# Kernel optimization log

Measured on AMD Instinct MI355X. Metric: run time of the kernel, lower is better.

The kernel has to match this reference:

```python
import jax, jax.numpy as jnp
import numpy as np

B, N, DIM = 16, 1024, 512
H, DH = 8, 64
INNER = H * DH            # 512
FF = 4 * DIM              # 2048
CIN = 2 * DIM             # conv inner dim = dim*expansion_factor = 1024
K = 31                    # depthwise kernel size
MAXPOS = 512
EPS = 1e-5


def layernorm(x, g, b):
    mu = jnp.mean(x, axis=-1, keepdims=True)
    var = jnp.mean(jnp.square(x - mu), axis=-1, keepdims=True)
    return (x - mu) * jax.lax.rsqrt(var + EPS) * g + b


def swish(x):
    return x * jax.nn.sigmoid(x)


def feed_forward(x, w1, b1, w2, b2):
    h = swish(x @ w1 + b1)
    return h @ w2 + b2


def setup_inputs() -> dict:
    key = jax.random.key(0)
    ks = jax.random.split(key, 16)
    s = 0.02
    w = lambda k, shape: (jax.random.normal(k, shape, jnp.float32) * s)
    inp = {
        "x": jax.random.normal(ks[0], (B, N, DIM), jnp.float32),
        # FF1
        "ff1_ln_g": jnp.ones((DIM,), jnp.float32), "ff1_ln_b": jnp.zeros((DIM,), jnp.float32),
        "ff1_w1": w(ks[1], (DIM, FF)), "ff1_b1": jnp.zeros((FF,), jnp.float32),
        "ff1_w2": w(ks[2], (FF, DIM)), "ff1_b2": jnp.zeros((DIM,), jnp.float32),
        # Attention (PreNorm)
        "attn_ln_g": jnp.ones((DIM,), jnp.float32), "attn_ln_b": jnp.zeros((DIM,), jnp.float32),
        "wq": w(ks[3], (DIM, INNER)),
        "wkv": w(ks[4], (DIM, 2 * INNER)),
        "wo": w(ks[5], (INNER, DIM)), "bo": jnp.zeros((DIM,), jnp.float32),
        "rel_emb": w(ks[6], (2 * MAXPOS + 1, DH)),
        # Conv module
        "conv_ln_g": jnp.ones((DIM,), jnp.float32), "conv_ln_b": jnp.zeros((DIM,), jnp.float32),
        "conv1_w": w(ks[7], (DIM, 2 * CIN)), "conv1_b": jnp.zeros((2 * CIN,), jnp.float32),
        "dw_w": w(ks[8], (CIN, 1, K)), "dw_b": jnp.zeros((CIN,), jnp.float32),
        "conv2_w": w(ks[9], (CIN, DIM)), "conv2_b": jnp.zeros((DIM,), jnp.float32),
        # FF2
        "ff2_ln_g": jnp.ones((DIM,), jnp.float32), "ff2_ln_b": jnp.zeros((DIM,), jnp.float32),
        "ff2_w1": w(ks[10], (DIM, FF)), "ff2_b1": jnp.zeros((FF,), jnp.float32),
        "ff2_w2": w(ks[11], (FF, DIM)), "ff2_b2": jnp.zeros((DIM,), jnp.float32),
        # post norm
        "post_ln_g": jnp.ones((DIM,), jnp.float32), "post_ln_b": jnp.zeros((DIM,), jnp.float32),
    }
    return inp


def attention(x, wq, wkv, wo, bo, rel_emb):
    b, n, _ = x.shape
    scale = DH ** -0.5
    q = (x @ wq).reshape(b, n, H, DH).transpose(0, 2, 1, 3)   # b h n d
    kv = x @ wkv
    k = kv[..., :INNER].reshape(b, n, H, DH).transpose(0, 2, 1, 3)
    v = kv[..., INNER:].reshape(b, n, H, DH).transpose(0, 2, 1, 3)
    dots = jnp.einsum("bhid,bhjd->bhij", q, k) * scale
    # relative positional bias via embedding lookup
    seq = jnp.arange(n)
    dist = jnp.clip(seq[:, None] - seq[None, :], -MAXPOS, MAXPOS) + MAXPOS  # [n, n]
    rel = jnp.take(rel_emb, dist, axis=0)                      # [n, n, d]
    pos = jnp.einsum("bhnd,njd->bhnj", q, rel) * scale
    attn = jax.nn.softmax(dots + pos, axis=-1)
    out = jnp.einsum("bhij,bhjd->bhid", attn, v)
    out = out.transpose(0, 2, 1, 3).reshape(b, n, INNER)
    return out @ wo + bo


def conv_module(x, ln_g, ln_b, conv1_w, conv1_b, dw_w, dw_b, conv2_w, conv2_b):
    h = layernorm(x, ln_g, ln_b)                               # [b, n, dim]
    h = h @ conv1_w + conv1_b                                  # pointwise conv -> [b, n, 2*CIN]
    a, g = h[..., :CIN], h[..., CIN:]
    h = a * jax.nn.sigmoid(g)                                  # GLU (channel dim)
    hc = h.transpose(0, 2, 1)                                  # [b, CIN, n]
    hc = jnp.pad(hc, ((0, 0), (0, 0), (K - 1, 0)))             # causal left pad
    hc = jax.lax.conv_general_dilated(
        hc, dw_w, window_strides=(1,), padding="VALID",
        feature_group_count=CIN, dimension_numbers=("NCH", "OIH", "NCH"),
    ) + dw_b[None, :, None]
    h = hc.transpose(0, 2, 1)                                  # [b, n, CIN]
    h = swish(h)
    return h @ conv2_w + conv2_b


def reference(x, ff1_ln_g, ff1_ln_b, ff1_w1, ff1_b1, ff1_w2, ff1_b2,
              attn_ln_g, attn_ln_b, wq, wkv, wo, bo, rel_emb,
              conv_ln_g, conv_ln_b, conv1_w, conv1_b, dw_w, dw_b, conv2_w, conv2_b,
              ff2_ln_g, ff2_ln_b, ff2_w1, ff2_b1, ff2_w2, ff2_b2,
              post_ln_g, post_ln_b):
    x = 0.5 * feed_forward(layernorm(x, ff1_ln_g, ff1_ln_b), ff1_w1, ff1_b1, ff1_w2, ff1_b2) + x
    x = attention(layernorm(x, attn_ln_g, attn_ln_b), wq, wkv, wo, bo, rel_emb) + x
    x = conv_module(x, conv_ln_g, conv_ln_b, conv1_w, conv1_b, dw_w, dw_b, conv2_w, conv2_b) + x
    x = 0.5 * feed_forward(layernorm(x, ff2_ln_g, ff2_ln_b), ff2_w1, ff2_b1, ff2_w2, ff2_b2) + x
    return layernorm(x, post_ln_g, post_ln_b)
```

## Files before the change

### kernel.cpp

```cpp
#include <hip/hip_runtime.h>


#define BN 16384

typedef unsigned short u16;
typedef __attribute__((ext_vector_type(8))) __bf16 bf16x8;
typedef __attribute__((ext_vector_type(4))) float f32x4;
typedef __attribute__((ext_vector_type(8))) unsigned short u16x8;

__device__ __forceinline__ float sigf(float x) { return 1.f / (1.f + __expf(-x)); }
__device__ __forceinline__ u16 f2bf(float f) {
  unsigned int u = __float_as_uint(f);
  u += 0x7FFF + ((u >> 16) & 1);
  return (u16)(u >> 16);
}
__device__ __forceinline__ u16 f2bfn(float f) {
  const __bf16 h = (__bf16)f;
  return __builtin_bit_cast(u16, h);
}
__device__ __forceinline__ float bf2f(u16 u) {
  return __uint_as_float(((unsigned int)u) << 16);
}
__device__ __forceinline__ void gl_lds16(const void* g, void* lds) {
  __builtin_amdgcn_global_load_lds(
      (const __attribute__((address_space(1))) unsigned int*)g,
      (__attribute__((address_space(3))) unsigned int*)lds, 16, 0, 0);
}

__global__ __launch_bounds__(256) void ln_kernel(const float* __restrict__ in,
    const float* __restrict__ g, const float* __restrict__ b,
    u16* outb, float* outf) {
  const int t = threadIdx.x;
  const int row = blockIdx.x * 2 + (t >> 7);
  const int tl = t & 127;
  const float4 v = ((const float4*)(in + (size_t)row * 512))[tl];
  float s = v.x + v.y + v.z + v.w;
  float sq = v.x * v.x + v.y * v.y + v.z * v.z + v.w * v.w;
#pragma unroll
  for (int o = 32; o > 0; o >>= 1) {
    s += __shfl_down(s, o);
    sq += __shfl_down(sq, o);
  }
  __shared__ float ss[4], ssq[4];
  if ((t & 63) == 0) { ss[t >> 6] = s; ssq[t >> 6] = sq; }
  __syncthreads();
  const int base = (t >> 7) * 2;
  s = ss[base] + ss[base + 1];
  sq = ssq[base] + ssq[base + 1];
  const float mu = s * (1.f / 512.f);
  const float var = fmaxf(sq * (1.f / 512.f) - mu * mu, 0.f);
  const float rstd = rsqrtf(var + 1e-5f);
  const float4 gg = ((const float4*)g)[tl];
  const float4 bb = ((const float4*)b)[tl];
  float o0 = (v.x - mu) * rstd * gg.x + bb.x;
  float o1 = (v.y - mu) * rstd * gg.y + bb.y;
  float o2 = (v.z - mu) * rstd * gg.z + bb.z;
  float o3 = (v.w - mu) * rstd * gg.w + bb.w;
  if (outf) {
    float4 o4 = {o0, o1, o2, o3};
    ((float4*)(outf + (size_t)row * 512))[tl] = o4;
  } else {
    ushort4 u4 = {f2bf(o0), f2bf(o1), f2bf(o2), f2bf(o3)};
    ((ushort4*)(outb + (size_t)row * 512))[tl] = u4;
  }
}

__global__ __launch_bounds__(256) void wtrans(const float* __restrict__ W,
                                              u16* __restrict__ WT, int K, int N) {
  const int n0 = blockIdx.x * 32, k0 = blockIdx.y * 32;
  const int t = threadIdx.x;
  const int tx = t & 31, ty = t >> 5;
  __shared__ float T[32][33];
#pragma unroll
  for (int i = 0; i < 4; ++i)
    T[tx][ty + 8 * i] = W[(size_t)(k0 + ty + 8 * i) * N + n0 + tx];
  __syncthreads();
#pragma unroll
  for (int i = 0; i < 4; ++i)
    WT[(size_t)(n0 + ty + 8 * i) * K + k0 + tx] = f2bf(T[ty + 8 * i][tx]);
}

__global__ __launch_bounds__(256) void cvt_bf16(const float* __restrict__ in,
                                                u16* __restrict__ out, int n) {
  const int i = blockIdx.x * 256 + threadIdx.x;
  if (i < n) out[i] = f2bf(in[i]);
}

__global__ __launch_bounds__(256) void gemm_bf16(const u16* __restrict__ A,
    const u16* __restrict__ WT, const float* __restrict__ bias,
    const float* res, float* Cf, u16* Cb, u16* VTout, int K, int N, int ldc,
    float alpha, int act, int qn, int vt0) {
  __shared__ __align__(16) u16 Ast[128 * 64];
  __shared__ __align__(16) u16 Bst[128 * 64];
  const int t = threadIdx.x;
  int bx = blockIdx.x, by = blockIdx.y;
  {
    const int nx = gridDim.x;
    const int lin = bx + nx * by;
    const int xcd = lin & 7;
    const int s = lin >> 3;
    const int ny8 = gridDim.y >> 3;
    const int sy = s / nx;
    by = xcd * ny8 + sy;
    bx = s - sy * nx;
  }
  const int n0 = bx * 128;
  const int m0 = by * 128;
  const int w = t >> 6;
  const int lc = t & 15, lq = (t >> 4) & 3;
  const int wy = w >> 1, wx = w & 1;
  f32x4 acc[4][4];
#pragma unroll
  for (int i = 0; i < 4; ++i)
#pragma unroll
    for (int j = 0; j < 4; ++j)
#pragma unroll
      for (int r = 0; r < 4; ++r) acc[i][j][r] = 0.f;

  const int koff0 = (lq ^ (lc & 7)) * 8;
  const int koff1 = ((4 + lq) ^ (lc & 7)) * 8;

  for (int kt = 0; kt < K; kt += 64) {
#pragma unroll
    for (int s = 0; s < 4; ++s) {
      const int f = t + 256 * s;
      const int fr = f >> 3;
      const int fc = (f & 7) ^ (fr & 7);
      gl_lds16(&A[(size_t)(m0 + fr) * K + kt + fc * 8], &Ast[f * 8]);
      gl_lds16(&WT[(size_t)(n0 + fr) * K + kt + fc * 8], &Bst[f * 8]);
    }
    __syncthreads();
#pragma unroll
    for (int kk = 0; kk < 2; ++kk) {
      const int koff = kk ? koff1 : koff0;
      bf16x8 bfr[4];
#pragma unroll
      for (int j = 0; j < 4; ++j)
        bfr[j] = *(const bf16x8*)&Bst[(wx * 64 + j * 16 + lc) * 64 + koff];
#pragma unroll
      for (int i = 0; i < 4; ++i) {
        const bf16x8 af = *(const bf16x8*)&Ast[(wy * 64 + i * 16 + lc) * 64 + koff];
#pragma unroll
        for (int j = 0; j < 4; ++j)
          acc[i][j] = __builtin_amdgcn_mfma_f32_16x16x32_bf16(af, bfr[j], acc[i][j], 0, 0, 0);
      }
    }
    __syncthreads();
  }

  const bool vtblk = (VTout != nullptr) && (n0 >= vt0);
  if (Cb && !vtblk) {
#pragma unroll
    for (int j = 0; j < 4; ++j) {
      const int coll = wx * 64 + j * 16 + lc;
      const float bj = bias ? bias[n0 + coll] : 0.f;
      const float al = ((n0 + coll) < qn) ? alpha : 1.f;
#pragma unroll
      for (int i = 0; i < 4; ++i) {
        const int rowl0 = wy * 64 + i * 16 + lq * 4;
#pragma unroll
        for (int r = 0; r < 4; ++r) {
          float v = acc[i][j][r] + bj;
          if (act) v = v * sigf(v);
          v *= al;
          const int rowl = rowl0 + r;
          u16* cl = (rowl < 64) ? &Ast[rowl * 128] : &Bst[(rowl - 64) * 128];
          cl[coll] = f2bfn(v);
        }
      }
    }
    __syncthreads();
#pragma unroll
    for (int vv = 0; vv < 8; ++vv) {
      const int e = t + 256 * vv;
      const int rowl = e >> 4;
      const int col = (e & 15) * 8;
      const u16* cl = (rowl < 64) ? &Ast[rowl * 128] : &Bst[(rowl - 64) * 128];
      const u16x8 val = *(const u16x8*)&cl[col];
      *(u16x8*)&Cb[(size_t)(m0 + rowl) * ldc + n0 + col] = val;
    }
    return;
  }

#pragma unroll
  for (int j = 0; j < 4; ++j) {
    const int col = n0 + wx * 64 + j * 16 + lc;
    const float bj = bias ? bias[col] : 0.f;
    const float al = (col < qn) ? alpha : 1.f;
    const bool vtc = vtblk && (col >= vt0);
#pragma unroll
    for (int i = 0; i < 4; ++i) {
      const int row0 = m0 + wy * 64 + i * 16 + lq * 4;
      float v4[4];
#pragma unroll
      for (int r = 0; r < 4; ++r) {
        float v = acc[i][j][r] + bj;
        if (act) v = v * sigf(v);
        v *= al;
        if (res) v += res[(size_t)(row0 + r) * ldc + col];
        v4[r] = v;
      }
      if (vtc) {
        const int cm = col - vt0;
        const int hh = cm >> 6, dd = cm & 63;
        const int bb = row0 >> 10, nl = row0 & 1023;
        ushort4 o4 = {f2bfn(v4[0]), f2bfn(v4[1]), f2bfn(v4[2]), f2bfn(v4[3])};
        *(ushort4*)&VTout[((size_t)((bb * 8 + hh) * 64 + dd)) * 1024 + nl] = o4;
      } else {
#pragma unroll
        for (int r = 0; r < 4; ++r) {
          const size_t off = (size_t)(row0 + r) * ldc + col;
          if (Cf) Cf[off] = v4[r];
          else Cb[off] = f2bfn(v4[r]);
        }
      }
    }
  }
}

__global__ __launch_bounds__(256) void attn_mfma(const u16* __restrict__ QKV,
    const u16* __restrict__ Vt, const u16* __restrict__ Rb, u16* __restrict__ O) {
  const int lin = blockIdx.x;
  const int hb = lin & 127;
  const int n0 = (lin >> 7) * 64;
  const int h = hb & 7, b = hb >> 3;
  const int t = threadIdx.x;
  const int w = t >> 6;
  const int lc = t & 15, lq = (t >> 4) & 3;

  __shared__ __align__(16) u16 Ks[2][64 * 64];
  __shared__ __align__(16) u16 Vs[2][64 * 64];
  __shared__ __align__(16) u16 SP[64 * 72];

  bf16x8 qf[2];
  {
    const size_t qrow = (size_t)(b * 1024 + n0 + w * 16 + lc) * 1536 + h * 64;
    qf[0] = *(const bf16x8*)&QKV[qrow + lq * 8];
    qf[1] = *(const bf16x8*)&QKV[qrow + 32 + lq * 8];
  }

  const u16* Kg = QKV + (size_t)b * 1024 * 1536 + 512 + h * 64;
  const u16* Vg = Vt + (size_t)(b * 8 + h) * 64 * 1024;

  const int srow = t >> 3;
  const int scb0 = ((t & 7) ^ (srow & 7)) * 8;
  const int srow1 = (t + 256) >> 3;
  const int scb1 = (((t + 256) & 7) ^ (srow1 & 7)) * 8;

  gl_lds16(&Kg[(size_t)srow * 1536 + scb0], &Ks[0][t * 8]);
  gl_lds16(&Vg[(size_t)srow * 1024 + scb0], &Vs[0][t * 8]);
  gl_lds16(&Kg[(size_t)srow1 * 1536 + scb1], &Ks[0][(t + 256) * 8]);
  gl_lds16(&Vg[(size_t)srow1 * 1024 + scb1], &Vs[0][(t + 256) * 8]);

  float l_r[4] = {0.f, 0.f, 0.f, 0.f};
  f32x4 o[4];
#pragma unroll
  for (int dt = 0; dt < 4; ++dt)
#pragma unroll
    for (int r = 0; r < 4; ++r) o[dt][r] = 0.f;

  const int swz0 = (lq ^ (lc & 7)) * 8;
  const int swz1 = ((4 + lq) ^ (lc & 7)) * 8;

  int buf = 0;
  for (int jt = 0; jt < 16; ++jt) {
    const int j0 = jt * 64;
    __syncthreads();

    if (jt < 15) {
      const int j1 = j0 + 64;
      gl_lds16(&Kg[(size_t)(j1 + srow) * 1536 + scb0], &Ks[buf ^ 1][t * 8]);
      gl_lds16(&Vg[(size_t)srow * 1024 + j1 + scb0], &Vs[buf ^ 1][t * 8]);
      gl_lds16(&Kg[(size_t)(j1 + srow1) * 1536 + scb1], &Ks[buf ^ 1][(t + 256) * 8]);
      gl_lds16(&Vg[(size_t)srow1 * 1024 + j1 + scb1], &Vs[buf ^ 1][(t + 256) * 8]);
    }

    f32x4 qk[4], pa[5];
#pragma unroll
    for (int j = 0; j < 4; ++j)
#pragma unroll
      for (int r = 0; r < 4; ++r) qk[j][r] = 0.f;
#pragma unroll
    for (int rtl = 0; rtl < 5; ++rtl)
#pragma unroll
      for (int r = 0; r < 4; ++r) pa[rtl][r] = 0.f;

    const int base = n0 - j0 - 63;
    const u16* rp[5];
#pragma unroll
    for (int rtl = 0; rtl < 5; ++rtl) {
      int p = base + (w + rtl) * 16 + lc;
      p = (p < -512 ? -512 : (p > 512 ? 512 : p)) + 512;
      rp[rtl] = Rb + (size_t)p * 64 + lq * 8;
    }

#pragma unroll
    for (int ks = 0; ks < 2; ++ks) {
      const int koff = ks ? swz1 : swz0;
      bf16x8 rfr[5];
#pragma unroll
      for (int rtl = 0; rtl < 5; ++rtl)
        rfr[rtl] = *(const bf16x8*)&rp[rtl][ks * 32];
#pragma unroll
      for (int j = 0; j < 4; ++j) {
        const bf16x8 bf = *(const bf16x8*)&Ks[buf][(j * 16 + lc) * 64 + koff];
        qk[j] = __builtin_amdgcn_mfma_f32_16x16x32_bf16(qf[ks], bf, qk[j], 0, 0, 0);
      }
#pragma unroll
      for (int rtl = 0; rtl < 5; ++rtl)
        pa[rtl] = __builtin_amdgcn_mfma_f32_16x16x32_bf16(qf[ks], rfr[rtl], pa[rtl], 0, 0, 0);
    }

#pragma unroll
    for (int rtl = 0; rtl < 5; ++rtl) {
      const int didx = (w + rtl) * 16 + lc;
#pragma unroll
      for (int r = 0; r < 4; ++r) {
        const int qr = w * 16 + lq * 4 + r;
        const int jc = qr - didx + 63;
        if ((unsigned)jc < 64u) SP[qr * 72 + jc] = f2bfn(pa[rtl][r]);
      }
    }

#pragma unroll
    for (int r = 0; r < 4; ++r) {
      const int qr = w * 16 + lq * 4 + r;
#pragma unroll
      for (int ti = 0; ti < 4; ++ti) {
        const int a = qr * 72 + ti * 16 + lc;
        const float e = exp2f(qk[ti][r] + bf2f(SP[a]));
        SP[a] = f2bfn(e);
        l_r[r] += e;
      }
    }

#pragma unroll
    for (int ks = 0; ks < 2; ++ks) {
      const bf16x8 af = *(const bf16x8*)&SP[(w * 16 + lc) * 72 + ks * 32 + lq * 8];
      const int koff = ks ? swz1 : swz0;
#pragma unroll
      for (int dt = 0; dt < 4; ++dt) {
        const bf16x8 bf = *(const bf16x8*)&Vs[buf][(dt * 16 + lc) * 64 + koff];
        o[dt] = __builtin_amdgcn_mfma_f32_16x16x32_bf16(af, bf, o[dt], 0, 0, 0);
      }
    }
    buf ^= 1;
  }

#pragma unroll
  for (int r = 0; r < 4; ++r) {
#pragma unroll
    for (int msk = 1; msk < 16; msk <<= 1) l_r[r] += __shfl_xor(l_r[r], msk);
  }

#pragma unroll
  for (int r = 0; r < 4; ++r) {
    const float inv = 1.f / l_r[r];
    const size_t row = (size_t)(b * 1024 + n0 + w * 16 + lq * 4 + r);
#pragma unroll
    for (int dt = 0; dt < 4; ++dt)
      O[row * 512 + h * 64 + dt * 16 + lc] = f2bfn(o[dt][r] * inv);
  }
}

__global__ __launch_bounds__(256) void dwconv_kernel(const u16* __restrict__ in,
    const float* __restrict__ w, const float* __restrict__ bias,
    u16* __restrict__ out) {
  const int n0 = blockIdx.x * 64;
  const int c0 = blockIdx.y * 64;
  const int b = blockIdx.z;
  const int t = threadIdx.x;
  __shared__ float hs[94][64];
  __shared__ float wsh[31][64];
  const int c = t & 63;
  const int g = t >> 6;
  for (int r = g; r < 94; r += 4) {
    const int n = n0 - 30 + r;
    float v = 0.f;
    if (n >= 0) {
      const size_t rowb = (size_t)(b * 1024 + n) * 2048;
      const float a = bf2f(in[rowb + c0 + c]);
      const float gg = bf2f(in[rowb + 1024 + c0 + c]);
      v = a * sigf(gg);
    }
    hs[r][c] = v;
  }
  for (int idx = t; idx < 31 * 64; idx += 256) {
    const int tap = idx >> 6, cc = idx & 63;
    wsh[tap][cc] = w[(size_t)(c0 + cc) * 31 + tap];
  }
  __syncthreads();
  float wr[31];
#pragma unroll
  for (int k = 0; k < 31; ++k) wr[k] = wsh[k][c];
  const float bsv = bias[c0 + c];
  float win[46];
  const int rbase = g * 16;
#pragma unroll
  for (int k = 0; k < 46; ++k) win[k] = hs[rbase + k][c];
#pragma unroll
  for (int i = 0; i < 16; ++i) {
    float acc = bsv;
#pragma unroll
    for (int k = 0; k < 31; ++k) acc += wr[k] * win[i + k];
    acc = acc * sigf(acc);
    out[(size_t)(b * 1024 + n0 + rbase + i) * 1024 + c0 + c] = f2bfn(acc);
  }
}

extern "C" void kernel_launch(void* const* d_in, const int* in_sizes, int n_in,
                              void* d_out, int out_size, void* d_ws, size_t ws_size,
                              hipStream_t stream) {
  const float* x        = (const float*)d_in[0];
  const float* ff1_ln_g = (const float*)d_in[1];
  const float* ff1_ln_b = (const float*)d_in[2];
  const float* ff1_w1   = (const float*)d_in[3];
  const float* ff1_b1   = (const float*)d_in[4];
  const float* ff1_w2   = (const float*)d_in[5];
  const float* ff1_b2   = (const float*)d_in[6];
  const float* attn_ln_g= (const float*)d_in[7];
  const float* attn_ln_b= (const float*)d_in[8];
  const float* wq       = (const float*)d_in[9];
  const float* wkv      = (const float*)d_in[10];
  const float* wo       = (const float*)d_in[11];
  const float* bo       = (const float*)d_in[12];
  const float* rel_emb  = (const float*)d_in[13];
  const float* conv_ln_g= (const float*)d_in[14];
  const float* conv_ln_b= (const float*)d_in[15];
  const float* conv1_w  = (const float*)d_in[16];
  const float* conv1_b  = (const float*)d_in[17];
  const float* dw_w     = (const float*)d_in[18];
  const float* dw_b     = (const float*)d_in[19];
  const float* conv2_w  = (const float*)d_in[20];
  const float* conv2_b  = (const float*)d_in[21];
  const float* ff2_ln_g = (const float*)d_in[22];
  const float* ff2_ln_b = (const float*)d_in[23];
  const float* ff2_w1   = (const float*)d_in[24];
  const float* ff2_b1   = (const float*)d_in[25];
  const float* ff2_w2   = (const float*)d_in[26];
  const float* ff2_b2   = (const float*)d_in[27];
  const float* post_ln_g= (const float*)d_in[28];
  const float* post_ln_b= (const float*)d_in[29];

  float* XRES = (float*)d_out;
  u16* ws = (u16*)d_ws;
  u16* LNB  = ws;
  u16* HID  = LNB + (size_t)BN * 512;
  u16* QKVB = HID + (size_t)BN * 2048;
  u16* VT   = QKVB + (size_t)BN * 1536;
  u16* DWB  = QKVB;
  u16* WTp = VT + (size_t)8192 * 1024;
  u16* wt_ff1w1 = WTp;                 WTp += (size_t)2048 * 512;
  u16* wt_ff1w2 = WTp;                 WTp += (size_t)512 * 2048;
  u16* wt_qkv   = WTp;                 WTp += (size_t)1536 * 512;
  u16* wt_wo    = WTp;                 WTp += (size_t)512 * 512;
  u16* wt_conv1 = WTp;                 WTp += (size_t)2048 * 512;
  u16* wt_conv2 = WTp;                 WTp += (size_t)512 * 1024;
  u16* wt_ff2w1 = WTp;                 WTp += (size_t)2048 * 512;
  u16* wt_ff2w2 = WTp;                 WTp += (size_t)512 * 2048;
  u16* RELB     = WTp;

  const dim3 blk(256);
  const float SC = 0.125f * 1.44269504f;

  wtrans<<<dim3(64, 16), blk, 0, stream>>>(ff1_w1, wt_ff1w1, 512, 2048);
  wtrans<<<dim3(16, 64), blk, 0, stream>>>(ff1_w2, wt_ff1w2, 2048, 512);
  wtrans<<<dim3(16, 16), blk, 0, stream>>>(wq, wt_qkv, 512, 512);
  wtrans<<<dim3(32, 16), blk, 0, stream>>>(wkv, wt_qkv + (size_t)512 * 512, 512, 1024);
  wtrans<<<dim3(16, 16), blk, 0, stream>>>(wo, wt_wo, 512, 512);
  wtrans<<<dim3(64, 16), blk, 0, stream>>>(conv1_w, wt_conv1, 512, 2048);
  wtrans<<<dim3(16, 32), blk, 0, stream>>>(conv2_w, wt_conv2, 1024, 512);
  wtrans<<<dim3(64, 16), blk, 0, stream>>>(ff2_w1, wt_ff2w1, 512, 2048);
  wtrans<<<dim3(16, 64), blk, 0, stream>>>(ff2_w2, wt_ff2w2, 2048, 512);
  cvt_bf16<<<257, blk, 0, stream>>>(rel_emb, RELB, 1025 * 64);

  ln_kernel<<<BN / 2, blk, 0, stream>>>(x, ff1_ln_g, ff1_ln_b, LNB, nullptr);
  gemm_bf16<<<dim3(16, 128), blk, 0, stream>>>(LNB, wt_ff1w1, ff1_b1, nullptr,
                                               nullptr, HID, nullptr, 512, 2048, 2048, 1.f, 1, 2048, 0);
  gemm_bf16<<<dim3(4, 128), blk, 0, stream>>>(HID, wt_ff1w2, ff1_b2, x,
                                              XRES, nullptr, nullptr, 2048, 512, 512, 0.5f, 0, 512, 0);

  ln_kernel<<<BN / 2, blk, 0, stream>>>(XRES, attn_ln_g, attn_ln_b, LNB, nullptr);
  gemm_bf16<<<dim3(12, 128), blk, 0, stream>>>(LNB, wt_qkv, nullptr, nullptr,
                                               nullptr, QKVB, VT, 512, 1536, 1536, SC, 0, 512, 1024);
  attn_mfma<<<dim3(2048), blk, 0, stream>>>(QKVB, VT, RELB, LNB);
  gemm_bf16<<<dim3(4, 128), blk, 0, stream>>>(LNB, wt_wo, bo, XRES,
                                              XRES, nullptr, nullptr, 512, 512, 512, 1.f, 0, 512, 0);

  ln_kernel<<<BN / 2, blk, 0, stream>>>(XRES, conv_ln_g, conv_ln_b, LNB, nullptr);
  gemm_bf16<<<dim3(16, 128), blk, 0, stream>>>(LNB, wt_conv1, conv1_b, nullptr,
                                               nullptr, HID, nullptr, 512, 2048, 2048, 1.f, 0, 2048, 0);
  dwconv_kernel<<<dim3(16, 16, 16), blk, 0, stream>>>(HID, dw_w, dw_b, DWB);
  gemm_bf16<<<dim3(4, 128), blk, 0, stream>>>(DWB, wt_conv2, conv2_b, XRES,
                                              XRES, nullptr, nullptr, 1024, 512, 512, 1.f, 0, 512, 0);

  ln_kernel<<<BN / 2, blk, 0, stream>>>(XRES, ff2_ln_g, ff2_ln_b, LNB, nullptr);
  gemm_bf16<<<dim3(16, 128), blk, 0, stream>>>(LNB, wt_ff2w1, ff2_b1, nullptr,
                                               nullptr, HID, nullptr, 512, 2048, 2048, 1.f, 1, 2048, 0);
  gemm_bf16<<<dim3(4, 128), blk, 0, stream>>>(HID, wt_ff2w2, ff2_b2, XRES,
                                              XRES, nullptr, nullptr, 2048, 512, 512, 0.5f, 0, 512, 0);

  ln_kernel<<<BN / 2, blk, 0, stream>>>(XRES, post_ln_g, post_ln_b, nullptr, XRES);
}
```

Measured before the change: 863.2 us.

## Add 256x256-tile double-buffered GEMM for the wide up-projection layers

Adds a new 512-thread GEMM kernel with 256x256 output tiles, 64-deep K slices double-buffered in 128KB of LDS, and an epilogue staged through LDS for coalesced 16-byte bf16 stores. It replaces the 128x128 gemm_bf16 for the three N=2048 up-projections (FF1, conv1, FF2). The aim is more operand reuse per byte loaded and overlap of global-to-LDS loads with MFMA work. In exchange, the full LDS use allows only one block per CU and needs many accumulator registers, and the grid of 512 blocks gives coarse wave quantization.

```diff
diff --git a/kernel.cpp b/kernel.cpp
--- a/kernel.cpp
+++ b/kernel.cpp
@@ -84,6 +84,110 @@
                                                 u16* __restrict__ out, int n) {
   const int i = blockIdx.x * 256 + threadIdx.x;
   if (i < n) out[i] = f2bf(in[i]);
+}
+
+__global__ __launch_bounds__(512) void gemm256(const u16* __restrict__ A,
+    const u16* __restrict__ WT, const float* __restrict__ bias,
+    u16* __restrict__ Cb, int K, int ldc, int act) {
+  __shared__ __align__(16) u16 LDSB[65536];
+  u16* const As0 = LDSB;
+  u16* const As1 = LDSB + 16384;
+  u16* const Bs0 = LDSB + 32768;
+  u16* const Bs1 = LDSB + 49152;
+  const int t = threadIdx.x;
+  int bx = blockIdx.x, by = blockIdx.y;
+  {
+    const int nx = gridDim.x;
+    const int lin = bx + nx * by;
+    const int xcd = lin & 7;
+    const int s = lin >> 3;
+    const int ny8 = gridDim.y >> 3;
+    const int sy = s / nx;
+    by = xcd * ny8 + sy;
+    bx = s - sy * nx;
+  }
+  const int n0 = bx * 256;
+  const int m0 = by * 256;
+  const int w = t >> 6;
+  const int wr = w >> 2, wc = w & 3;
+  const int lc = t & 15, lq = (t >> 4) & 3;
+
+  f32x4 acc[8][4];
+#pragma unroll
+  for (int i = 0; i < 8; ++i)
+#pragma unroll
+    for (int j = 0; j < 4; ++j)
+#pragma unroll
+      for (int r = 0; r < 4; ++r) acc[i][j][r] = 0.f;
+
+  int sfr[4], sfc[4];
+#pragma unroll
+  for (int s = 0; s < 4; ++s) {
+    const int f = t + 512 * s;
+    sfr[s] = f >> 3;
+    sfc[s] = ((f & 7) ^ (sfr[s] & 7)) * 8;
+  }
+
+  auto STAGE = [&](u16* Ad, u16* Bd, int kt) {
+#pragma unroll
+    for (int s = 0; s < 4; ++s) {
+      gl_lds16(&A[(size_t)(m0 + sfr[s]) * K + kt + sfc[s]], &Ad[(t + 512 * s) * 8]);
+      gl_lds16(&WT[(size_t)(n0 + sfr[s]) * K + kt + sfc[s]], &Bd[(t + 512 * s) * 8]);
+    }
+  };
+
+  auto COMPUTE = [&](const u16* Asrc, const u16* Bsrc) {
+#pragma unroll
+    for (int kk = 0; kk < 2; ++kk) {
+      const int koff = ((kk * 4 + lq) ^ (lc & 7)) * 8;
+      bf16x8 bfr[4];
+#pragma unroll
+      for (int j = 0; j < 4; ++j)
+        bfr[j] = *(const bf16x8*)&Bsrc[(wc * 64 + j * 16 + lc) * 64 + koff];
+#pragma unroll
+      for (int i = 0; i < 8; ++i) {
+        const bf16x8 af = *(const bf16x8*)&Asrc[(wr * 128 + i * 16 + lc) * 64 + koff];
+#pragma unroll
+        for (int j = 0; j < 4; ++j)
+          acc[i][j] = __builtin_amdgcn_mfma_f32_16x16x32_bf16(af, bfr[j], acc[i][j], 0, 0, 0);
+      }
+    }
+  };
+
+  STAGE(As0, Bs0, 0);
+  __syncthreads();
+
+  for (int kt2 = 0; kt2 < K; kt2 += 128) {
+    STAGE(As1, Bs1, kt2 + 64);
+    COMPUTE(As0, Bs0);
+    __syncthreads();
+    if (kt2 + 128 < K) STAGE(As0, Bs0, kt2 + 128);
+    COMPUTE(As1, Bs1);
+    __syncthreads();
+  }
+
+#pragma unroll
+  for (int j = 0; j < 4; ++j) {
+    const int coll = wc * 64 + j * 16 + lc;
+    const float bj = bias[n0 + coll];
+#pragma unroll
+    for (int i = 0; i < 8; ++i) {
+      const int rowl0 = wr * 128 + i * 16 + lq * 4;
+#pragma unroll
+      for (int r = 0; r < 4; ++r) {
+        float v = acc[i][j][r] + bj;
+        if (act) v = v * sigf(v);
+        LDSB[(rowl0 + r) * 256 + coll] = f2bfn(v);
+      }
+    }
+  }
+  __syncthreads();
+#pragma unroll
+  for (int vv = 0; vv < 16; ++vv) {
+    const int e = t + 512 * vv;
+    *(u16x8*)&Cb[(size_t)(m0 + (e >> 5)) * ldc + n0 + (e & 31) * 8] =
+        *(const u16x8*)&LDSB[e * 8];
+  }
 }
 
 __global__ __launch_bounds__(256) void gemm_bf16(const u16* __restrict__ A,
@@ -475,8 +579,7 @@
   cvt_bf16<<<257, blk, 0, stream>>>(rel_emb, RELB, 1025 * 64);
 
   ln_kernel<<<BN / 2, blk, 0, stream>>>(x, ff1_ln_g, ff1_ln_b, LNB, nullptr);
-  gemm_bf16<<<dim3(16, 128), blk, 0, stream>>>(LNB, wt_ff1w1, ff1_b1, nullptr,
-                                               nullptr, HID, nullptr, 512, 2048, 2048, 1.f, 1, 2048, 0);
+  gemm256<<<dim3(8, 64), dim3(512), 0, stream>>>(LNB, wt_ff1w1, ff1_b1, HID, 512, 2048, 1);
   gemm_bf16<<<dim3(4, 128), blk, 0, stream>>>(HID, wt_ff1w2, ff1_b2, x,
                                               XRES, nullptr, nullptr, 2048, 512, 512, 0.5f, 0, 512, 0);
 
@@ -488,15 +591,13 @@
                                               XRES, nullptr, nullptr, 512, 512, 512, 1.f, 0, 512, 0);
 
   ln_kernel<<<BN / 2, blk, 0, stream>>>(XRES, conv_ln_g, conv_ln_b, LNB, nullptr);
-  gemm_bf16<<<dim3(16, 128), blk, 0, stream>>>(LNB, wt_conv1, conv1_b, nullptr,
-                                               nullptr, HID, nullptr, 512, 2048, 2048, 1.f, 0, 2048, 0);
+  gemm256<<<dim3(8, 64), dim3(512), 0, stream>>>(LNB, wt_conv1, conv1_b, HID, 512, 2048, 0);
   dwconv_kernel<<<dim3(16, 16, 16), blk, 0, stream>>>(HID, dw_w, dw_b, DWB);
   gemm_bf16<<<dim3(4, 128), blk, 0, stream>>>(DWB, wt_conv2, conv2_b, XRES,
                                               XRES, nullptr, nullptr, 1024, 512, 512, 1.f, 0, 512, 0);
 
   ln_kernel<<<BN / 2, blk, 0, stream>>>(XRES, ff2_ln_g, ff2_ln_b, LNB, nullptr);
-  gemm_bf16<<<dim3(16, 128), blk, 0, stream>>>(LNB, wt_ff2w1, ff2_b1, nullptr,
-                                               nullptr, HID, nullptr, 512, 2048, 2048, 1.f, 1, 2048, 0);
+  gemm256<<<dim3(8, 64), dim3(512), 0, stream>>>(LNB, wt_ff2w1, ff2_b1, HID, 512, 2048, 1);
   gemm_bf16<<<dim3(4, 128), blk, 0, stream>>>(HID, wt_ff2w2, ff2_b2, XRES,
                                               XRES, nullptr, nullptr, 2048, 512, 512, 0.5f, 0, 512, 0);
 
```

Result: no change. 862.7 us (-0.1%).
